# Kernel tuning notes

Hardware: AMD Instinct MI355X
Metric: run time of the kernel (lower is better)

Reference implementation:

```python
import jax, jax.numpy as jnp
import numpy as np

B, D, H = 8192, 512, 512


def _linear_init(key, out_dim, in_dim, bias=True):
    # torch nn.Linear default: U(-1/sqrt(in_dim), 1/sqrt(in_dim)) for W and b
    k1, k2 = jax.random.split(key)
    bound = 1.0 / np.sqrt(in_dim)
    W = jax.random.uniform(k1, (out_dim, in_dim), jnp.float32, -bound, bound)
    if not bias:
        return W
    b = jax.random.uniform(k2, (out_dim,), jnp.float32, -bound, bound)
    return W, b


def setup_inputs() -> dict:
    key = jax.random.key(0)
    ks = jax.random.split(key, 16)
    x = jax.random.normal(ks[0], (B, D), jnp.float32)
    delta_t = jax.random.uniform(ks[1], (B, 1), jnp.float32)
    hidden = jax.random.normal(ks[2], (B, H), jnp.float32)
    cell_s = jax.random.normal(ks[3], (B, H), jnp.float32)
    Wii, bii = _linear_init(ks[4], H, D)
    Whi, bhi = _linear_init(ks[5], H, H)
    Wig, big = _linear_init(ks[6], H, D)
    Whg, bhg = _linear_init(ks[7], H, H)
    Wio, bio = _linear_init(ks[8], H, D)
    Who, bho = _linear_init(ks[9], H, H)
    Wto, bto = _linear_init(ks[10], H, 1)
    Wco, bco = _linear_init(ks[11], H, H)
    Wit1, bit1 = _linear_init(ks[12], H, D)
    Wtt1 = _linear_init(ks[13], H, 1, bias=False)
    Wit2, bit2 = _linear_init(ks[14], H, D)
    Wtt2 = _linear_init(ks[15], H, 1, bias=False)
    return dict(x=x, delta_t=delta_t, hidden=hidden, cell_s=cell_s,
                Wii=Wii, bii=bii, Whi=Whi, bhi=bhi, Wig=Wig, big=big,
                Whg=Whg, bhg=bhg, Wio=Wio, bio=bio, Who=Who, bho=bho,
                Wto=Wto, bto=bto, Wco=Wco, bco=bco, Wit1=Wit1, bit1=bit1,
                Wtt1=Wtt1, Wit2=Wit2, bit2=bit2, Wtt2=Wtt2)


def _lin(a, W, b=None):
    y = a @ W.T
    return y if b is None else y + b


def reference(x, delta_t, hidden, cell_s,
              Wii, bii, Whi, bhi, Wig, big, Whg, bhg,
              Wio, bio, Who, bho, Wto, bto, Wco, bco,
              Wit1, bit1, Wtt1, Wit2, bit2, Wtt2):
    sig, tanh = jax.nn.sigmoid, jnp.tanh
    tm1 = sig(_lin(x, Wit1, bit1) + sig(_lin(delta_t, Wtt1)))
    tm2 = sig(_lin(x, Wit2, bit2) + sig(_lin(delta_t, Wtt2)))
    im = sig(_lin(x, Wii, bii) + _lin(hidden, Whi, bhi))
    cur_in = tanh(_lin(x, Wig, big) + _lin(hidden, Whg, bhg))
    it1 = im * tm1
    cm_t = (1.0 - it1) * cell_s + it1 * cur_in
    cm = (1.0 - im) * cell_s + im * tm2 * cur_in
    om = sig(_lin(x, Wio, bio) + _lin(delta_t, Wto, bto)
             + _lin(hidden, Who, bho) + _lin(cm_t, Wco, bco))
    hm = om * tanh(cm_t)
    return (hm, cm)
```

## Files before the change

kernel.cpp:

```cpp
#include <hip/hip_runtime.h>
#include <hip/hip_bf16.h>
#include <stdint.h>

#define B_SZ 8192
#define D_SZ 512
#define H_SZ 512
#define KC 1024
#define NPRE 2560
#define PRE_LD 2560

typedef __attribute__((ext_vector_type(8))) __bf16 bf16x8;
typedef __attribute__((ext_vector_type(4))) float f32x4;

__device__ __forceinline__ unsigned short f2bf(float f) {
  unsigned u = __builtin_bit_cast(unsigned, f);
  u += 0x7FFFu + ((u >> 16) & 1u);
  return (unsigned short)(u >> 16);
}
__device__ __forceinline__ float bf2f(unsigned short h) {
  unsigned u = ((unsigned)h) << 16;
  return __builtin_bit_cast(float, u);
}
__device__ __forceinline__ float sigf(float x) { return 1.0f / (1.0f + __expf(-x)); }

__device__ __forceinline__ void async_ld16(const unsigned short* g, unsigned short* l) {
  __builtin_amdgcn_global_load_lds(
      (const __attribute__((address_space(1))) unsigned int*)g,
      (__attribute__((address_space(3))) unsigned int*)l, 16, 0, 0);
}

__global__ void pack_xh(const float* __restrict__ x, const float* __restrict__ h,
                        unsigned short* __restrict__ Ab) {
  int i = (blockIdx.x * 256 + threadIdx.x) * 4;
  int b = i >> 10, c = i & 1023;
  const float* s = (c < 512) ? (x + (size_t)b * 512 + c)
                             : (h + (size_t)b * 512 + (c - 512));
  float4 v = *(const float4*)s;
  ushort4 o; o.x = f2bf(v.x); o.y = f2bf(v.y); o.z = f2bf(v.z); o.w = f2bf(v.w);
  *(ushort4*)(Ab + i) = o;
}

struct WSrcs { const float* wx[5]; const float* wh[3]; const float* wco; };

__global__ void pack_w(WSrcs ws, unsigned short* __restrict__ Wall,
                       unsigned short* __restrict__ Wcob) {
  int i = (blockIdx.x * 256 + threadIdx.x) * 4;
  if (i < NPRE * KC) {
    int row = i >> 10, c = i & 1023;
    int gate = row >> 9, r = row & 511;
    ushort4 o;
    if (c < 512) {
      float4 v = *(const float4*)(ws.wx[gate] + (size_t)r * 512 + c);
      o.x = f2bf(v.x); o.y = f2bf(v.y); o.z = f2bf(v.z); o.w = f2bf(v.w);
    } else if (gate >= 2) {
      float4 v = *(const float4*)(ws.wh[gate - 2] + (size_t)r * 512 + (c - 512));
      o.x = f2bf(v.x); o.y = f2bf(v.y); o.z = f2bf(v.z); o.w = f2bf(v.w);
    } else {
      o.x = 0; o.y = 0; o.z = 0; o.w = 0;
    }
    *(ushort4*)(Wall + i) = o;
  } else {
    int j = i - NPRE * KC;
    float4 v = *(const float4*)(ws.wco + j);
    ushort4 o; o.x = f2bf(v.x); o.y = f2bf(v.y); o.z = f2bf(v.z); o.w = f2bf(v.w);
    *(ushort4*)(Wcob + j) = o;
  }
}

__global__ __launch_bounds__(256, 2) void gemm_bt(
    const unsigned short* __restrict__ A, const unsigned short* __restrict__ W,
    unsigned short* __restrict__ C, int K, int ldc) {
  __shared__ bf16x8 sA[128 * 8];
  __shared__ bf16x8 sW[128 * 8];
  const int tid  = threadIdx.x;
  const int wave = tid >> 6, lane = tid & 63;
  const int ln15 = lane & 15, kq = lane >> 4;
  const int wr = wave >> 1, wc = wave & 1;
  const long bm = (long)blockIdx.y * 128;
  const long bn = (long)blockIdx.x * 128;

  f32x4 acc[4][4];
#pragma unroll
  for (int i = 0; i < 4; ++i)
#pragma unroll
    for (int j = 0; j < 4; ++j) acc[i][j] = (f32x4){0.f, 0.f, 0.f, 0.f};

  const int nK = K >> 6;
  for (int kt = 0; kt < nK; ++kt) {
    const int k0 = kt << 6;
    __syncthreads();
#pragma unroll
    for (int it = 0; it < 4; ++it) {
      int f   = it * 256 + tid;
      int row = f >> 3;
      int col = (f & 7) << 3;
      int ldsc = it * 256 + wave * 64;
      async_ld16(A + (size_t)(bm + row) * K + k0 + col, (unsigned short*)sA + (size_t)ldsc * 8);
      async_ld16(W + (size_t)(bn + row) * K + k0 + col, (unsigned short*)sW + (size_t)ldsc * 8);
    }
    __syncthreads();
#pragma unroll
    for (int ko = 0; ko < 2; ++ko) {
      bf16x8 af[4], wf[4];
#pragma unroll
      for (int t = 0; t < 4; ++t)
        af[t] = sA[(wr * 64 + t * 16 + ln15) * 8 + ko * 4 + kq];
#pragma unroll
      for (int t = 0; t < 4; ++t)
        wf[t] = sW[(wc * 64 + t * 16 + ln15) * 8 + ko * 4 + kq];
#pragma unroll
      for (int i = 0; i < 4; ++i)
#pragma unroll
        for (int j = 0; j < 4; ++j)
          acc[i][j] = __builtin_amdgcn_mfma_f32_16x16x32_bf16(af[i], wf[j], acc[i][j], 0, 0, 0);
    }
  }
#pragma unroll
  for (int i = 0; i < 4; ++i) {
    const long r0 = bm + wr * 64 + i * 16 + kq * 4;
#pragma unroll
    for (int j = 0; j < 4; ++j) {
      const long c = bn + wc * 64 + j * 16 + ln15;
#pragma unroll
      for (int r = 0; r < 4; ++r)
        C[(size_t)(r0 + r) * ldc + c] = f2bf(acc[i][j][r]);
    }
  }
}

__global__ void gate_kernel(unsigned short* __restrict__ Pre,
                            const float* __restrict__ delta_t, const float* __restrict__ cell_s,
                            const float* __restrict__ bii, const float* __restrict__ bhi,
                            const float* __restrict__ big, const float* __restrict__ bhg,
                            const float* __restrict__ bio, const float* __restrict__ bho,
                            const float* __restrict__ Wto, const float* __restrict__ bto,
                            const float* __restrict__ bco,
                            const float* __restrict__ bit1, const float* __restrict__ Wtt1,
                            const float* __restrict__ bit2, const float* __restrict__ Wtt2,
                            float* __restrict__ out_cm, unsigned short* __restrict__ cmt_b) {
  int i4 = (blockIdx.x * 256 + threadIdx.x) * 4;
  int b = i4 >> 9, h = i4 & 511;
  size_t p = (size_t)b * PRE_LD;
  float dt = delta_t[b];
  ushort4 u1 = *(const ushort4*)(Pre + p + h);
  ushort4 u2 = *(const ushort4*)(Pre + p + 512 + h);
  ushort4 ui = *(const ushort4*)(Pre + p + 1024 + h);
  ushort4 ug = *(const ushort4*)(Pre + p + 1536 + h);
  ushort4 uo = *(const ushort4*)(Pre + p + 2048 + h);
  float4 cs  = *(const float4*)(cell_s + i4);
  float4 vbii = *(const float4*)(bii + h),  vbhi = *(const float4*)(bhi + h);
  float4 vbig = *(const float4*)(big + h),  vbhg = *(const float4*)(bhg + h);
  float4 vbio = *(const float4*)(bio + h),  vbho = *(const float4*)(bho + h);
  float4 vWto = *(const float4*)(Wto + h),  vbto = *(const float4*)(bto + h);
  float4 vbco = *(const float4*)(bco + h);
  float4 vbt1 = *(const float4*)(bit1 + h), vwt1 = *(const float4*)(Wtt1 + h);
  float4 vbt2 = *(const float4*)(bit2 + h), vwt2 = *(const float4*)(Wtt2 + h);

  float4 ocm; ushort4 ocmt; ushort4 oao;
  const unsigned short* pu1 = (const unsigned short*)&u1;
  const unsigned short* pu2 = (const unsigned short*)&u2;
  const unsigned short* pui = (const unsigned short*)&ui;
  const unsigned short* pug = (const unsigned short*)&ug;
  const unsigned short* puo = (const unsigned short*)&uo;
  const float* pcs = (const float*)&cs;
  float* pocm = (float*)&ocm;
  unsigned short* pocmt = (unsigned short*)&ocmt;
  unsigned short* poao = (unsigned short*)&oao;
#pragma unroll
  for (int l = 0; l < 4; ++l) {
    float a1 = bf2f(pu1[l]) + ((const float*)&vbt1)[l];
    float a2 = bf2f(pu2[l]) + ((const float*)&vbt2)[l];
    float ai = bf2f(pui[l]) + ((const float*)&vbii)[l] + ((const float*)&vbhi)[l];
    float ag = bf2f(pug[l]) + ((const float*)&vbig)[l] + ((const float*)&vbhg)[l];
    float ao = bf2f(puo[l]) + ((const float*)&vbio)[l] + ((const float*)&vbho)[l]
             + dt * ((const float*)&vWto)[l] + ((const float*)&vbto)[l] + ((const float*)&vbco)[l];
    float t1 = sigf(a1 + sigf(dt * ((const float*)&vwt1)[l]));
    float t2 = sigf(a2 + sigf(dt * ((const float*)&vwt2)[l]));
    float im = sigf(ai);
    float g  = tanhf(ag);
    float csl = pcs[l];
    float it1 = im * t1;
    float cmt = (1.f - it1) * csl + it1 * g;
    float cm  = (1.f - im) * csl + im * t2 * g;
    pocm[l]  = cm;
    pocmt[l] = f2bf(cmt);
    poao[l]  = f2bf(ao);
  }
  *(float4*)(out_cm + i4) = ocm;
  *(ushort4*)(cmt_b + i4) = ocmt;
  *(ushort4*)(Pre + p + 2048 + h) = oao;
}

__global__ __launch_bounds__(256, 2) void gemm_out(
    const unsigned short* __restrict__ A , const unsigned short* __restrict__ W ,
    const unsigned short* __restrict__ Pre, float* __restrict__ out_hm) {
  __shared__ bf16x8 sA[128 * 8];
  __shared__ bf16x8 sW[128 * 8];
  const int tid  = threadIdx.x;
  const int wave = tid >> 6, lane = tid & 63;
  const int ln15 = lane & 15, kq = lane >> 4;
  const int wr = wave >> 1, wc = wave & 1;
  const long bm = (long)blockIdx.y * 128;
  const long bn = (long)blockIdx.x * 128;
  const int K = H_SZ;

  f32x4 acc[4][4];
#pragma unroll
  for (int i = 0; i < 4; ++i)
#pragma unroll
    for (int j = 0; j < 4; ++j) acc[i][j] = (f32x4){0.f, 0.f, 0.f, 0.f};

  for (int kt = 0; kt < (K >> 6); ++kt) {
    const int k0 = kt << 6;
    __syncthreads();
#pragma unroll
    for (int it = 0; it < 4; ++it) {
      int f   = it * 256 + tid;
      int row = f >> 3;
      int col = (f & 7) << 3;
      int ldsc = it * 256 + wave * 64;
      async_ld16(A + (size_t)(bm + row) * K + k0 + col, (unsigned short*)sA + (size_t)ldsc * 8);
      async_ld16(W + (size_t)(bn + row) * K + k0 + col, (unsigned short*)sW + (size_t)ldsc * 8);
    }
    __syncthreads();
#pragma unroll
    for (int ko = 0; ko < 2; ++ko) {
      bf16x8 af[4], wf[4];
#pragma unroll
      for (int t = 0; t < 4; ++t)
        af[t] = sA[(wr * 64 + t * 16 + ln15) * 8 + ko * 4 + kq];
#pragma unroll
      for (int t = 0; t < 4; ++t)
        wf[t] = sW[(wc * 64 + t * 16 + ln15) * 8 + ko * 4 + kq];
#pragma unroll
      for (int i = 0; i < 4; ++i)
#pragma unroll
        for (int j = 0; j < 4; ++j)
          acc[i][j] = __builtin_amdgcn_mfma_f32_16x16x32_bf16(af[i], wf[j], acc[i][j], 0, 0, 0);
    }
  }
#pragma unroll
  for (int i = 0; i < 4; ++i) {
    const long r0 = bm + wr * 64 + i * 16 + kq * 4;
#pragma unroll
    for (int j = 0; j < 4; ++j) {
      const long c = bn + wc * 64 + j * 16 + ln15;
#pragma unroll
      for (int r = 0; r < 4; ++r) {
        long row = r0 + r;
        size_t idx = (size_t)row * H_SZ + c;
        float ao  = bf2f(Pre[(size_t)row * PRE_LD + 2048 + c]);
        float om  = sigf(ao + acc[i][j][r]);
        float cmt = bf2f(A[idx]);
        out_hm[idx] = om * tanhf(cmt);
      }
    }
  }
}

extern "C" void kernel_launch(void* const* d_in, const int* in_sizes, int n_in,
                              void* d_out, int out_size, void* d_ws, size_t ws_size,
                              hipStream_t stream) {
  const float* x    = (const float*)d_in[0];
  const float* dt   = (const float*)d_in[1];
  const float* hid  = (const float*)d_in[2];
  const float* cell = (const float*)d_in[3];
  const float* Wii  = (const float*)d_in[4];
  const float* bii  = (const float*)d_in[5];
  const float* Whi  = (const float*)d_in[6];
  const float* bhi  = (const float*)d_in[7];
  const float* Wig  = (const float*)d_in[8];
  const float* big  = (const float*)d_in[9];
  const float* Whg  = (const float*)d_in[10];
  const float* bhg  = (const float*)d_in[11];
  const float* Wio  = (const float*)d_in[12];
  const float* bio  = (const float*)d_in[13];
  const float* Who  = (const float*)d_in[14];
  const float* bho  = (const float*)d_in[15];
  const float* Wto  = (const float*)d_in[16];
  const float* bto  = (const float*)d_in[17];
  const float* Wco  = (const float*)d_in[18];
  const float* bco  = (const float*)d_in[19];
  const float* Wit1 = (const float*)d_in[20];
  const float* bit1 = (const float*)d_in[21];
  const float* Wtt1 = (const float*)d_in[22];
  const float* Wit2 = (const float*)d_in[23];
  const float* bit2 = (const float*)d_in[24];
  const float* Wtt2 = (const float*)d_in[25];

  char* wp = (char*)d_ws;
  unsigned short* Ab   = (unsigned short*)wp; wp += (size_t)B_SZ * KC * 2;
  unsigned short* Wall = (unsigned short*)wp; wp += (size_t)NPRE * KC * 2;
  unsigned short* Wcob = (unsigned short*)wp; wp += (size_t)H_SZ * H_SZ * 2;
  unsigned short* Pre  = (unsigned short*)wp; wp += (size_t)B_SZ * PRE_LD * 2;
  unsigned short* Cmtb = (unsigned short*)wp; wp += (size_t)B_SZ * H_SZ * 2;

  float* out = (float*)d_out;

  pack_xh<<<(B_SZ * KC) / 4 / 256, 256, 0, stream>>>(x, hid, Ab);
  WSrcs wsrc;
  wsrc.wx[0] = Wit1; wsrc.wx[1] = Wit2; wsrc.wx[2] = Wii; wsrc.wx[3] = Wig; wsrc.wx[4] = Wio;
  wsrc.wh[0] = Whi;  wsrc.wh[1] = Whg;  wsrc.wh[2] = Who; wsrc.wco = Wco;
  pack_w<<<(NPRE * KC + H_SZ * H_SZ) / 4 / 256, 256, 0, stream>>>(wsrc, Wall, Wcob);

  gemm_bt<<<dim3(NPRE / 128, B_SZ / 128), 256, 0, stream>>>(Ab, Wall, Pre, KC, PRE_LD);

  gate_kernel<<<(B_SZ * H_SZ) / 4 / 256, 256, 0, stream>>>(
      Pre, dt, cell, bii, bhi, big, bhg, bio, bho, Wto, bto, bco, bit1, Wtt1, bit2, Wtt2,
      out + (size_t)B_SZ * H_SZ, Cmtb);

  gemm_out<<<dim3(H_SZ / 128, B_SZ / 128), 256, 0, stream>>>(Cmtb, Wcob, Pre, out);
}
```

Measured before the change: 251.6 us.

## Swizzle LDS tiles, skip zero-weight K half, and merge pack kernels

Applies an XOR swizzle to the LDS layout in both GEMM kernels so the 16-byte fragment reads stop hitting the same banks. In gemm_bt, column blocks covering the first 1024 outputs (the time-gate weights whose hidden half is zero-padded) now loop over only K=512, skipping MFMA work on known zeros. The two pack kernels become one launch, removing a kernel dispatch. The K-skip relies on the zero padding of Wall staying in place.

```diff
diff --git a/kernel.cpp b/kernel.cpp
--- a/kernel.cpp
+++ b/kernel.cpp
@@ -29,42 +29,40 @@
       (__attribute__((address_space(3))) unsigned int*)l, 16, 0, 0);
 }
 
-__global__ void pack_xh(const float* __restrict__ x, const float* __restrict__ h,
-                        unsigned short* __restrict__ Ab) {
+struct WSrcs { const float* wx[5]; const float* wh[3]; const float* wco; };
+
+__global__ void pack_all(const float* __restrict__ x, const float* __restrict__ h, WSrcs ws,
+                         unsigned short* __restrict__ Ab, unsigned short* __restrict__ Wall,
+                         unsigned short* __restrict__ Wcob) {
   int i = (blockIdx.x * 256 + threadIdx.x) * 4;
-  int b = i >> 10, c = i & 1023;
-  const float* s = (c < 512) ? (x + (size_t)b * 512 + c)
-                             : (h + (size_t)b * 512 + (c - 512));
+  const int XH = B_SZ * KC;
+  const float* s;
+  unsigned short* d;
+  if (i < XH) {
+    int b = i >> 10, c = i & 1023;
+    s = (c < 512) ? (x + (size_t)b * 512 + c) : (h + (size_t)b * 512 + (c - 512));
+    d = Ab + i;
+  } else if (i < XH + NPRE * KC) {
+    int j = i - XH;
+    int row = j >> 10, c = j & 1023;
+    int gate = row >> 9, r = row & 511;
+    d = Wall + j;
+    if (c < 512) {
+      s = ws.wx[gate] + (size_t)r * 512 + c;
+    } else if (gate >= 2) {
+      s = ws.wh[gate - 2] + (size_t)r * 512 + (c - 512);
+    } else {
+      *(ushort4*)d = (ushort4){0, 0, 0, 0};
+      return;
+    }
+  } else {
+    int j = i - XH - NPRE * KC;
+    s = ws.wco + j;
+    d = Wcob + j;
+  }
   float4 v = *(const float4*)s;
   ushort4 o; o.x = f2bf(v.x); o.y = f2bf(v.y); o.z = f2bf(v.z); o.w = f2bf(v.w);
-  *(ushort4*)(Ab + i) = o;
-}
-
-struct WSrcs { const float* wx[5]; const float* wh[3]; const float* wco; };
-
-__global__ void pack_w(WSrcs ws, unsigned short* __restrict__ Wall,
-                       unsigned short* __restrict__ Wcob) {
-  int i = (blockIdx.x * 256 + threadIdx.x) * 4;
-  if (i < NPRE * KC) {
-    int row = i >> 10, c = i & 1023;
-    int gate = row >> 9, r = row & 511;
-    ushort4 o;
-    if (c < 512) {
-      float4 v = *(const float4*)(ws.wx[gate] + (size_t)r * 512 + c);
-      o.x = f2bf(v.x); o.y = f2bf(v.y); o.z = f2bf(v.z); o.w = f2bf(v.w);
-    } else if (gate >= 2) {
-      float4 v = *(const float4*)(ws.wh[gate - 2] + (size_t)r * 512 + (c - 512));
-      o.x = f2bf(v.x); o.y = f2bf(v.y); o.z = f2bf(v.z); o.w = f2bf(v.w);
-    } else {
-      o.x = 0; o.y = 0; o.z = 0; o.w = 0;
-    }
-    *(ushort4*)(Wall + i) = o;
-  } else {
-    int j = i - NPRE * KC;
-    float4 v = *(const float4*)(ws.wco + j);
-    ushort4 o; o.x = f2bf(v.x); o.y = f2bf(v.y); o.z = f2bf(v.z); o.w = f2bf(v.w);
-    *(ushort4*)(Wcob + j) = o;
-  }
+  *(ushort4*)d = o;
 }
 
 __global__ __launch_bounds__(256, 2) void gemm_bt(
@@ -85,7 +83,9 @@
 #pragma unroll
     for (int j = 0; j < 4; ++j) acc[i][j] = (f32x4){0.f, 0.f, 0.f, 0.f};
 
-  const int nK = K >> 6;
+  const int nK = (bn < 1024) ? (512 >> 6) : (K >> 6);
+  const int swb = ln15 & 7;
+
   for (int kt = 0; kt < nK; ++kt) {
     const int k0 = kt << 6;
     __syncthreads();
@@ -93,7 +93,7 @@
     for (int it = 0; it < 4; ++it) {
       int f   = it * 256 + tid;
       int row = f >> 3;
-      int col = (f & 7) << 3;
+      int col = ((f & 7) ^ (row & 7)) << 3;
       int ldsc = it * 256 + wave * 64;
       async_ld16(A + (size_t)(bm + row) * K + k0 + col, (unsigned short*)sA + (size_t)ldsc * 8);
       async_ld16(W + (size_t)(bn + row) * K + k0 + col, (unsigned short*)sW + (size_t)ldsc * 8);
@@ -101,13 +101,14 @@
     __syncthreads();
 #pragma unroll
     for (int ko = 0; ko < 2; ++ko) {
+      const int q = (ko * 4 + kq) ^ swb;
       bf16x8 af[4], wf[4];
 #pragma unroll
       for (int t = 0; t < 4; ++t)
-        af[t] = sA[(wr * 64 + t * 16 + ln15) * 8 + ko * 4 + kq];
+        af[t] = sA[(wr * 64 + t * 16 + ln15) * 8 + q];
 #pragma unroll
       for (int t = 0; t < 4; ++t)
-        wf[t] = sW[(wc * 64 + t * 16 + ln15) * 8 + ko * 4 + kq];
+        wf[t] = sW[(wc * 64 + t * 16 + ln15) * 8 + q];
 #pragma unroll
       for (int i = 0; i < 4; ++i)
 #pragma unroll
@@ -203,6 +204,7 @@
   const long bm = (long)blockIdx.y * 128;
   const long bn = (long)blockIdx.x * 128;
   const int K = H_SZ;
+  const int swb = ln15 & 7;
 
   f32x4 acc[4][4];
 #pragma unroll
@@ -217,7 +219,7 @@
     for (int it = 0; it < 4; ++it) {
       int f   = it * 256 + tid;
       int row = f >> 3;
-      int col = (f & 7) << 3;
+      int col = ((f & 7) ^ (row & 7)) << 3;
       int ldsc = it * 256 + wave * 64;
       async_ld16(A + (size_t)(bm + row) * K + k0 + col, (unsigned short*)sA + (size_t)ldsc * 8);
       async_ld16(W + (size_t)(bn + row) * K + k0 + col, (unsigned short*)sW + (size_t)ldsc * 8);
@@ -225,13 +227,14 @@
     __syncthreads();
 #pragma unroll
     for (int ko = 0; ko < 2; ++ko) {
+      const int q = (ko * 4 + kq) ^ swb;
       bf16x8 af[4], wf[4];
 #pragma unroll
       for (int t = 0; t < 4; ++t)
-        af[t] = sA[(wr * 64 + t * 16 + ln15) * 8 + ko * 4 + kq];
+        af[t] = sA[(wr * 64 + t * 16 + ln15) * 8 + q];
 #pragma unroll
       for (int t = 0; t < 4; ++t)
-        wf[t] = sW[(wc * 64 + t * 16 + ln15) * 8 + ko * 4 + kq];
+        wf[t] = sW[(wc * 64 + t * 16 + ln15) * 8 + q];
 #pragma unroll
       for (int i = 0; i < 4; ++i)
 #pragma unroll
@@ -297,11 +300,11 @@
 
   float* out = (float*)d_out;
 
-  pack_xh<<<(B_SZ * KC) / 4 / 256, 256, 0, stream>>>(x, hid, Ab);
   WSrcs wsrc;
   wsrc.wx[0] = Wit1; wsrc.wx[1] = Wit2; wsrc.wx[2] = Wii; wsrc.wx[3] = Wig; wsrc.wx[4] = Wio;
   wsrc.wh[0] = Whi;  wsrc.wh[1] = Whg;  wsrc.wh[2] = Who; wsrc.wco = Wco;
-  pack_w<<<(NPRE * KC + H_SZ * H_SZ) / 4 / 256, 256, 0, stream>>>(wsrc, Wall, Wcob);
+  const int pack_elems = B_SZ * KC + NPRE * KC + H_SZ * H_SZ;
+  pack_all<<<pack_elems / 4 / 256, 256, 0, stream>>>(x, hid, wsrc, Ab, Wall, Wcob);
 
   gemm_bt<<<dim3(NPRE / 128, B_SZ / 128), 256, 0, stream>>>(Ab, Wall, Pre, KC, PRE_LD);
 
```

Result: faster. 233.9 us (-7.0%).
